# Kernel tuning notes

Measured on AMD Instinct MI355X. Metric: run time of the kernel, lower is better.

## Reference

```python
import jax, jax.numpy as jnp
import numpy as np

N = 100000   # total nodes (types a: [0,50000), b: [50000,100000))
E = 500000   # edges per edge type
T = 4        # number of edge types
D_IN = 128
H = 4        # heads
F = 32       # out_feats per head
NEG_SLOPE = 0.2


def setup_inputs() -> dict:
    key = jax.random.key(0)
    ks = jax.random.split(key, 8)
    feat = jax.random.normal(ks[0], (N, D_IN), dtype=jnp.float32)
    src = jax.random.randint(ks[1], (T, E), 0, N)
    dst = jax.random.randint(ks[2], (T, E), 0, N)
    is_b = jnp.arange(N) >= (N // 2)  # node-type mask (type2mask)
    W = jax.random.normal(ks[3], (T, D_IN, H * F), dtype=jnp.float32) * (1.0 / np.sqrt(D_IN))
    attn_l = jax.random.normal(ks[4], (T, H, F), dtype=jnp.float32) * 0.1
    attn_r = jax.random.normal(ks[5], (T, H, F), dtype=jnp.float32) * 0.1
    W_merge = jax.random.normal(ks[6], (2 * H * F, F), dtype=jnp.float32) * (1.0 / np.sqrt(2 * H * F))
    b_merge = jax.random.normal(ks[7], (F,), dtype=jnp.float32) * 0.01
    return {"feat": feat, "src": src, "dst": dst, "is_b": is_b,
            "W": W, "attn_l": attn_l, "attn_r": attn_r,
            "W_merge": W_merge, "b_merge": b_merge}


def _gat_etype(feat, src_t, dst_t, W_t, al_t, ar_t):
    # Projected features: [N, H, F]
    ft = (feat @ W_t).reshape(N, H, F)
    el = jnp.einsum('nhf,hf->nh', ft, al_t)  # [N, H]
    er = jnp.einsum('nhf,hf->nh', ft, ar_t)  # [N, H]
    # u_add_v then LeakyReLU: [E, H]
    e = el[src_t] + er[dst_t]
    e = jnp.where(e > 0, e, NEG_SLOPE * e)
    # edge_softmax over incoming edges of each dst node (stable)
    m = jax.lax.stop_gradient(jax.ops.segment_max(e, dst_t, num_segments=N))
    ex = jnp.exp(e - m[dst_t])
    denom = jax.ops.segment_sum(ex, dst_t, num_segments=N)
    a = ex / denom[dst_t]  # [E, H]
    # u_mul_e + scatter-sum: [N, H, F]
    msg = ft[src_t] * a[:, :, None]
    out = jax.ops.segment_sum(msg, dst_t, num_segments=N)
    return out.reshape(N, H * F)


def reference(feat, src, dst, is_b, W, attn_l, attn_r, W_merge, b_merge):
    outs = [_gat_etype(feat, src[t], dst[t], W[t], attn_l[t], attn_r[t])
            for t in range(T)]
    # etypes dst order: a, a, b, b -> two per-etype feats per dst ntype
    feat_a = jnp.concatenate([outs[0], outs[1]], axis=1) @ W_merge + b_merge  # [N, F]
    feat_b = jnp.concatenate([outs[2], outs[3]], axis=1) @ W_merge + b_merge  # [N, F]
    # base_aggr_func: start with type-a result, overwrite type-b rows
    return jnp.where(is_b[:, None], feat_b, feat_a)
```

## Files before the change

### kernel.cpp

```cpp
#include <hip/hip_runtime.h>
#include <hip/hip_fp16.h>

typedef short short8 __attribute__((ext_vector_type(8)));
typedef _Float16 half8 __attribute__((ext_vector_type(8)));
typedef float f32x4 __attribute__((ext_vector_type(4)));

#define N_NODES 100000
#define N_A     50000
#define N_EDGES 500000
#define N_T     4
#define D_IN    128
#define HF      128
#define BCOLS   144
#define TN      (N_T * N_NODES)
#define TE      (N_T * N_EDGES)
#define NB1     ((TN + 1023) / 1024)
#define TILE_E  (BCOLS * D_IN)
#define LOG2E   1.44269504088896340736f

__device__ __forceinline__ unsigned short f2b(float f) {
  unsigned int u = __float_as_uint(f);
  u += 0x7FFFu + ((u >> 16) & 1u);
  return (unsigned short)(u >> 16);
}
__device__ __forceinline__ unsigned int pkh(float lo, float hi) {
  auto v = __builtin_amdgcn_cvt_pkrtz(lo, hi);
  unsigned int u; __builtin_memcpy(&u, &v, 4); return u;
}
__device__ __forceinline__ unsigned short f2h(float f) {
  auto v = __builtin_amdgcn_cvt_pkrtz(f, 0.f);
  unsigned int u; __builtin_memcpy(&u, &v, 4); return (unsigned short)(u & 0xFFFFu);
}
__device__ __forceinline__ __half2 w2h(unsigned int u) {
  __half2 h; __builtin_memcpy(&h, &u, 4); return h;
}
__device__ __forceinline__ unsigned int h2w(__half2 h) {
  unsigned int u; __builtin_memcpy(&u, &h, 4); return u;
}

__global__ __launch_bounds__(256) void k_prep(const float* __restrict__ W,
    const float* __restrict__ al, const float* __restrict__ ar,
    const float* __restrict__ Wm,
    unsigned short* __restrict__ Bt, unsigned short* __restrict__ WmT)
{
  if (blockIdx.x < 2) {
    int idx = blockIdx.x * 256 + threadIdx.x;
    int t = idx >> 7, k = idx & 127;
    const float* Wr = W + ((size_t)t * D_IN + k) * HF;
    unsigned short* o = Bt + (size_t)t * TILE_E;
    for (int j = 0; j < HF; ++j)
      o[(j * D_IN + k) ^ ((j & 7) << 3)] = f2b(Wr[j]);
    for (int h = 0; h < 4; ++h) {
      float sl = 0.f, sr = 0.f;
      const float* alh = al + (t * 4 + h) * 32;
      const float* arh = ar + (t * 4 + h) * 32;
      for (int f = 0; f < 32; ++f) { float w = Wr[h * 32 + f]; sl += w * alh[f]; sr += w * arh[f]; }
      int jl = 128 + h, jr = 132 + h;
      o[(jl * D_IN + k) ^ ((jl & 7) << 3)] = f2b(sl * LOG2E);
      o[(jr * D_IN + k) ^ ((jr & 7) << 3)] = f2b(sr * LOG2E);
    }
    for (int j = 136; j < 144; ++j)
      o[(j * D_IN + k) ^ ((j & 7) << 3)] = 0;
  } else {
    int idx = (blockIdx.x - 2) * 256 + threadIdx.x;
    int kidx = idx >> 5, j = idx & 31;
    int slot = kidx >> 7, p = kidx & 127;
    int col = (p & 7) * 16 + (p >> 3);
    WmT[j * 256 + kidx] = f2h(Wm[(slot * 128 + col) * 32 + j]);
  }
}

__global__ __launch_bounds__(256, 4) void k_proj(const float* __restrict__ feat,
    const unsigned short* __restrict__ Btg,
    unsigned short* __restrict__ ftg,
    float* __restrict__ elg, float* __restrict__ erg)
{
  __shared__ __align__(16) unsigned short Bs[TILE_E];
  const int tid = threadIdx.x;
  const int wave = tid >> 6, lane = tid & 63;
  const int l15 = lane & 15, g = lane >> 4;
  const int wrow0 = blockIdx.x * 64 + wave * 16;

  short8 a[4];
  {
    int row = wrow0 + l15;
    const float* fr = feat + (size_t)(row < N_NODES ? row : N_NODES - 1) * D_IN;
#pragma unroll
    for (int kt = 0; kt < 4; ++kt) {
      float4 v0 = *(const float4*)(fr + kt * 32 + g * 8);
      float4 v1 = *(const float4*)(fr + kt * 32 + g * 8 + 4);
      short8 s;
      s[0] = (short)f2b(v0.x); s[1] = (short)f2b(v0.y);
      s[2] = (short)f2b(v0.z); s[3] = (short)f2b(v0.w);
      s[4] = (short)f2b(v1.x); s[5] = (short)f2b(v1.y);
      s[6] = (short)f2b(v1.z); s[7] = (short)f2b(v1.w);
      a[kt] = s;
    }
  }

  for (int t = 0; t < N_T; ++t) {
    if (t > 0) __syncthreads();
    {
      const uint4* src = (const uint4*)(Btg + (size_t)t * TILE_E);
      uint4* dstv = (uint4*)Bs;
#pragma unroll
      for (int i = 0; i < 9; ++i)
        dstv[i * 256 + tid] = src[i * 256 + tid];
    }
    __syncthreads();

    f32x4 acc[8];
#pragma unroll
    for (int ct = 0; ct < 8; ++ct) {
      f32x4 c = {0.f, 0.f, 0.f, 0.f};
#pragma unroll
      for (int kt = 0; kt < 4; ++kt) {
        int row = ct * 16 + l15;
        int boff = (row * 256 + kt * 64 + g * 16) ^ ((l15 & 7) << 4);
        short8 b = *(const short8*)((const char*)Bs + boff);
        c = __builtin_amdgcn_mfma_f32_16x16x32_bf16(a[kt], b, c, 0, 0, 0);
      }
      acc[ct] = c;
    }
    {
      f32x4 c8 = {0.f, 0.f, 0.f, 0.f};
#pragma unroll
      for (int kt = 0; kt < 4; ++kt) {
        int row = 128 + l15;
        int boff = (row * 256 + kt * 64 + g * 16) ^ ((l15 & 7) << 4);
        short8 b = *(const short8*)((const char*)Bs + boff);
        c8 = __builtin_amdgcn_mfma_f32_16x16x32_bf16(a[kt], b, c8, 0, 0, 0);
      }
      if (l15 < 8) {
#pragma unroll
        for (int r = 0; r < 4; ++r) {
          int row = wrow0 + g * 4 + r;
          if (row < N_NODES) {
            float v = c8[r];
            if (l15 < 4) elg[((size_t)t * N_NODES + row) * 4 + l15] = v;
            else         erg[((size_t)t * N_NODES + row) * 4 + (l15 - 4)] = v;
          }
        }
      }
    }
#pragma unroll
    for (int r = 0; r < 4; ++r) {
      int row = wrow0 + g * 4 + r;
      if (row < N_NODES) {
        uint4 o;
        o.x = pkh(acc[0][r], acc[1][r]);
        o.y = pkh(acc[2][r], acc[3][r]);
        o.z = pkh(acc[4][r], acc[5][r]);
        o.w = pkh(acc[6][r], acc[7][r]);
        *(uint4*)(ftg + ((size_t)t * N_NODES + row) * HF + l15 * 8) = o;
      }
    }
  }
}

__global__ __launch_bounds__(256) void k_hist(const int* __restrict__ dst,
    int* __restrict__ cnt, int* __restrict__ rank) {
  int idx = blockIdx.x * 256 + threadIdx.x;
  if (idx >= TE) return;
  int t = idx / N_EDGES;
  int d = dst[idx];
  bool keep = (t < 2) ? (d < N_A) : (d >= N_A);
  if (keep) rank[idx] = atomicAdd(&cnt[t * N_NODES + d], 1);
}

__global__ __launch_bounds__(256) void k_scan1(const int* __restrict__ cnt,
    int* __restrict__ ofs, int* __restrict__ bsum) {
  __shared__ int ts[256];
  int b = blockIdx.x, t = threadIdx.x;
  int base = b * 1024 + t * 4;
  int v0 = 0, v1 = 0, v2 = 0, v3 = 0;
  if (base + 0 < TN) v0 = cnt[base + 0];
  if (base + 1 < TN) v1 = cnt[base + 1];
  if (base + 2 < TN) v2 = cnt[base + 2];
  if (base + 3 < TN) v3 = cnt[base + 3];
  int s = v0 + v1 + v2 + v3;
  ts[t] = s;
  __syncthreads();
  for (int o = 1; o < 256; o <<= 1) {
    int x = (t >= o) ? ts[t - o] : 0;
    __syncthreads();
    ts[t] += x;
    __syncthreads();
  }
  int run = ts[t] - s;
  if (base + 0 < TN) ofs[base + 0] = run; run += v0;
  if (base + 1 < TN) ofs[base + 1] = run; run += v1;
  if (base + 2 < TN) ofs[base + 2] = run; run += v2;
  if (base + 3 < TN) ofs[base + 3] = run;
  if (t == 255) bsum[b] = ts[255];
}

__global__ __launch_bounds__(512) void k_scan2(int* __restrict__ bsum) {
  __shared__ int ts[512];
  int t = threadIdx.x;
  int v = (t < NB1) ? bsum[t] : 0;
  ts[t] = v;
  __syncthreads();
  for (int o = 1; o < 512; o <<= 1) {
    int x = (t >= o) ? ts[t - o] : 0;
    __syncthreads();
    ts[t] += x;
    __syncthreads();
  }
  if (t < NB1) bsum[t] = ts[t] - v;
}

__global__ __launch_bounds__(256) void k_scatter(const int* __restrict__ src, const int* __restrict__ dst,
    const int* __restrict__ ofs, const int* __restrict__ bsum, const int* __restrict__ rank,
    int* __restrict__ bkt) {
  int idx = blockIdx.x * 256 + threadIdx.x;
  if (idx >= TE) return;
  int t = idx / N_EDGES;
  int d = dst[idx];
  bool keep = (t < 2) ? (d < N_A) : (d >= N_A);
  if (!keep) return;
  int key = t * N_NODES + d;
  int p = ofs[key] + bsum[key >> 10] + rank[idx];
  bkt[p] = t * N_NODES + src[idx];
}

__global__ __launch_bounds__(256) void k_gathermerge(const int* __restrict__ bkt,
    const int* __restrict__ ofs, const int* __restrict__ cnt, const int* __restrict__ bsum,
    const float* __restrict__ elg, const float* __restrict__ erg,
    const uint4* __restrict__ ftu,
    const unsigned short* __restrict__ WmT, const float* __restrict__ bm,
    float* __restrict__ out)
{
  __shared__ __align__(16) unsigned short Al[16 * 264];
  int tid = threadIdx.x;
  int wave = tid >> 6, lane = tid & 63;
  int g8 = lane >> 3, l7 = lane & 7;
  int pidl = wave * 8 + g8;
  int pid = blockIdx.x * 32 + pidl;
  int n = pid >> 1, slot = pid & 1;
  int t = slot + ((n >= N_A) ? 2 : 0);
  int key = t * N_NODES + n;
  int base = ofs[key] + bsum[key >> 10];
  int c = cnt[key];
  float4 er4 = *(const float4*)(erg + (size_t)key * 4);
  __half2 A0 = __float2half2_rn(0.f), A1 = A0, A2 = A0, A3 = A0;
  __half2 B0 = A0, B1 = A0, B2 = A0, B3 = A0;
  float d0 = 0.f, d1 = 0.f, d2 = 0.f, d3 = 0.f;
  int qb = l7 * 2;
  for (int i = 0; i < c; i += 4) {
    bool v1 = i + 1 < c, v2 = i + 2 < c, v3 = i + 3 < c;
    int e0 = base + i;
    int e1 = base + (v1 ? i + 1 : i);
    int e2 = base + (v2 ? i + 2 : i);
    int e3 = base + (v3 ? i + 3 : i);
    int s0 = bkt[e0], s1 = bkt[e1], s2 = bkt[e2], s3 = bkt[e3];
    float4 eA = *(const float4*)(elg + (size_t)s0 * 4);
    float4 eB = *(const float4*)(elg + (size_t)s1 * 4);
    float4 eC = *(const float4*)(elg + (size_t)s2 * 4);
    float4 eD = *(const float4*)(elg + (size_t)s3 * 4);
    uint4 u0a = ftu[(size_t)s0 * 16 + qb], u0b = ftu[(size_t)s0 * 16 + qb + 1];
    uint4 u1a = ftu[(size_t)s1 * 16 + qb], u1b = ftu[(size_t)s1 * 16 + qb + 1];
    uint4 u2a = ftu[(size_t)s2 * 16 + qb], u2b = ftu[(size_t)s2 * 16 + qb + 1];
    uint4 u3a = ftu[(size_t)s3 * 16 + qb], u3b = ftu[(size_t)s3 * 16 + qb + 1];
    float s;
    float wa0, wa1, wa2, wa3, wb0, wb1, wb2, wb3;
    float wc0, wc1, wc2, wc3, wd0, wd1, wd2, wd3;
    s = eA.x + er4.x; wa0 = exp2f(fmaxf(s, 0.2f * s));
    s = eA.y + er4.y; wa1 = exp2f(fmaxf(s, 0.2f * s));
    s = eA.z + er4.z; wa2 = exp2f(fmaxf(s, 0.2f * s));
    s = eA.w + er4.w; wa3 = exp2f(fmaxf(s, 0.2f * s));
    s = eB.x + er4.x; wb0 = exp2f(fmaxf(s, 0.2f * s));
    s = eB.y + er4.y; wb1 = exp2f(fmaxf(s, 0.2f * s));
    s = eB.z + er4.z; wb2 = exp2f(fmaxf(s, 0.2f * s));
    s = eB.w + er4.w; wb3 = exp2f(fmaxf(s, 0.2f * s));
    s = eC.x + er4.x; wc0 = exp2f(fmaxf(s, 0.2f * s));
    s = eC.y + er4.y; wc1 = exp2f(fmaxf(s, 0.2f * s));
    s = eC.z + er4.z; wc2 = exp2f(fmaxf(s, 0.2f * s));
    s = eC.w + er4.w; wc3 = exp2f(fmaxf(s, 0.2f * s));
    s = eD.x + er4.x; wd0 = exp2f(fmaxf(s, 0.2f * s));
    s = eD.y + er4.y; wd1 = exp2f(fmaxf(s, 0.2f * s));
    s = eD.z + er4.z; wd2 = exp2f(fmaxf(s, 0.2f * s));
    s = eD.w + er4.w; wd3 = exp2f(fmaxf(s, 0.2f * s));
    if (!v1) { wb0 = wb1 = wb2 = wb3 = 0.f; }
    if (!v2) { wc0 = wc1 = wc2 = wc3 = 0.f; }
    if (!v3) { wd0 = wd1 = wd2 = wd3 = 0.f; }
    d0 += wa0 + wb0 + wc0 + wd0;
    d1 += wa1 + wb1 + wc1 + wd1;
    d2 += wa2 + wb2 + wc2 + wd2;
    d3 += wa3 + wb3 + wc3 + wd3;
    __half2 h0, h1, h2, h3;
    h0 = __float2half2_rn(wa0); h1 = __float2half2_rn(wa1);
    h2 = __float2half2_rn(wa2); h3 = __float2half2_rn(wa3);
    A0 = __hfma2(w2h(u0a.x), h0, A0); A1 = __hfma2(w2h(u0a.y), h1, A1);
    A2 = __hfma2(w2h(u0a.z), h2, A2); A3 = __hfma2(w2h(u0a.w), h3, A3);
    B0 = __hfma2(w2h(u0b.x), h0, B0); B1 = __hfma2(w2h(u0b.y), h1, B1);
    B2 = __hfma2(w2h(u0b.z), h2, B2); B3 = __hfma2(w2h(u0b.w), h3, B3);
    h0 = __float2half2_rn(wb0); h1 = __float2half2_rn(wb1);
    h2 = __float2half2_rn(wb2); h3 = __float2half2_rn(wb3);
    A0 = __hfma2(w2h(u1a.x), h0, A0); A1 = __hfma2(w2h(u1a.y), h1, A1);
    A2 = __hfma2(w2h(u1a.z), h2, A2); A3 = __hfma2(w2h(u1a.w), h3, A3);
    B0 = __hfma2(w2h(u1b.x), h0, B0); B1 = __hfma2(w2h(u1b.y), h1, B1);
    B2 = __hfma2(w2h(u1b.z), h2, B2); B3 = __hfma2(w2h(u1b.w), h3, B3);
    h0 = __float2half2_rn(wc0); h1 = __float2half2_rn(wc1);
    h2 = __float2half2_rn(wc2); h3 = __float2half2_rn(wc3);
    A0 = __hfma2(w2h(u2a.x), h0, A0); A1 = __hfma2(w2h(u2a.y), h1, A1);
    A2 = __hfma2(w2h(u2a.z), h2, A2); A3 = __hfma2(w2h(u2a.w), h3, A3);
    B0 = __hfma2(w2h(u2b.x), h0, B0); B1 = __hfma2(w2h(u2b.y), h1, B1);
    B2 = __hfma2(w2h(u2b.z), h2, B2); B3 = __hfma2(w2h(u2b.w), h3, B3);
    h0 = __float2half2_rn(wd0); h1 = __float2half2_rn(wd1);
    h2 = __float2half2_rn(wd2); h3 = __float2half2_rn(wd3);
    A0 = __hfma2(w2h(u3a.x), h0, A0); A1 = __hfma2(w2h(u3a.y), h1, A1);
    A2 = __hfma2(w2h(u3a.z), h2, A2); A3 = __hfma2(w2h(u3a.w), h3, A3);
    B0 = __hfma2(w2h(u3b.x), h0, B0); B1 = __hfma2(w2h(u3b.y), h1, B1);
    B2 = __hfma2(w2h(u3b.z), h2, B2); B3 = __hfma2(w2h(u3b.w), h3, B3);
  }
  __half2 i0 = __float2half2_rn((c > 0) ? 1.f / d0 : 0.f);
  __half2 i1 = __float2half2_rn((c > 0) ? 1.f / d1 : 0.f);
  __half2 i2 = __float2half2_rn((c > 0) ? 1.f / d2 : 0.f);
  __half2 i3 = __float2half2_rn((c > 0) ? 1.f / d3 : 0.f);
  uint4 oA, oB;
  oA.x = h2w(__hmul2(A0, i0)); oA.y = h2w(__hmul2(A1, i1));
  oA.z = h2w(__hmul2(A2, i2)); oA.w = h2w(__hmul2(A3, i3));
  oB.x = h2w(__hmul2(B0, i0)); oB.y = h2w(__hmul2(B1, i1));
  oB.z = h2w(__hmul2(B2, i2)); oB.w = h2w(__hmul2(B3, i3));
  int nl = pidl >> 1;
  *(uint4*)&Al[nl * 264 + slot * 128 + l7 * 16] = oA;
  *(uint4*)&Al[nl * 264 + slot * 128 + l7 * 16 + 8] = oB;
  __syncthreads();
  if (wave >= 2) return;

  int l15 = lane & 15, lk = (lane >> 4) * 8;
  f32x4 acc = {0.f, 0.f, 0.f, 0.f};
#pragma unroll
  for (int kt = 0; kt < 8; ++kt) {
    half8 a = *(const half8*)&Al[l15 * 264 + kt * 32 + lk];
    half8 b = *(const half8*)(const void*)(WmT + (size_t)(wave * 16 + l15) * 256 + kt * 32 + lk);
    acc = __builtin_amdgcn_mfma_f32_16x16x32_f16(a, b, acc, 0, 0, 0);
  }
  float bmv = bm[wave * 16 + l15];
#pragma unroll
  for (int r = 0; r < 4; ++r) {
    int row = blockIdx.x * 16 + (lane >> 4) * 4 + r;
    out[(size_t)row * 32 + wave * 16 + l15] = acc[r] + bmv;
  }
}

extern "C" void kernel_launch(void* const* d_in, const int* in_sizes, int n_in,
                              void* d_out, int out_size, void* d_ws, size_t ws_size,
                              hipStream_t stream)
{
  const float* feat = (const float*)d_in[0];
  const int*   src  = (const int*)d_in[1];
  const int*   dst  = (const int*)d_in[2];
  const float* W    = (const float*)d_in[4];
  const float* al   = (const float*)d_in[5];
  const float* ar   = (const float*)d_in[6];
  const float* Wm   = (const float*)d_in[7];
  const float* bm   = (const float*)d_in[8];
  float* out = (float*)d_out;
  (void)in_sizes; (void)n_in; (void)out_size; (void)ws_size;

  char* w = (char*)d_ws;
  size_t o = 0;
  auto take = [&](size_t bytes) -> void* {
    void* p = w + o;
    o += (bytes + 255) & ~(size_t)255;
    return p;
  };
  unsigned short* Btg = (unsigned short*)take((size_t)N_T * TILE_E * 2);
  unsigned short* WmT = (unsigned short*)take((size_t)32 * 256 * 2);
  unsigned short* ftg = (unsigned short*)take((size_t)N_T * N_NODES * HF * 2);
  float* elg   = (float*)take((size_t)N_T * N_NODES * 4 * 4);
  float* erg   = (float*)take((size_t)N_T * N_NODES * 4 * 4);
  int*   cntb  = (int*)take((size_t)TN * 4);
  int*   ofs   = (int*)take((size_t)TN * 4);
  int*   bsum  = (int*)take(4096);
  int*   rank  = (int*)take((size_t)TE * 4);
  int*   bkt   = (int*)take((size_t)TE * 4);

  hipMemsetAsync(cntb, 0, (size_t)TN * 4, stream);

  k_prep<<<34, 256, 0, stream>>>(W, al, ar, Wm, Btg, WmT);
  k_proj<<<1563, 256, 0, stream>>>(feat, Btg, ftg, elg, erg);
  k_hist<<<(TE + 255) / 256, 256, 0, stream>>>(dst, cntb, rank);
  k_scan1<<<NB1, 256, 0, stream>>>(cntb, ofs, bsum);
  k_scan2<<<1, 512, 0, stream>>>(bsum);
  k_scatter<<<(TE + 255) / 256, 256, 0, stream>>>(src, dst, ofs, bsum, rank, bkt);
  k_gathermerge<<<6250, 256, 0, stream>>>(bkt, ofs, cntb, bsum, elg, erg,
                                          (const uint4*)ftg, WmT, bm, out);
}
```

Measured before the change: 187.7 us.

## Fuse histogram, scans and scatter into one cooperative kernel; zero counts in prep

Replaces the four edge-bucketing kernels (hist, scan1, scan2, scatter) with a single cooperative kernel of 2048 blocks that uses grid-wide syncs between phases. The count buffer is now zeroed inside k_prep instead of with a separate memset. The aim is to cut launch overhead and inter-kernel gaps, at the price of grid.sync barriers and a grid-stride loop over fewer threads. The second-level scan now runs in one 256-thread block with two elements per thread.

```diff
diff --git a/kernel.cpp b/kernel.cpp
--- a/kernel.cpp
+++ b/kernel.cpp
@@ -1,5 +1,8 @@
 #include <hip/hip_runtime.h>
 #include <hip/hip_fp16.h>
+#include <hip/hip_cooperative_groups.h>
+
+namespace cg = cooperative_groups;
 
 typedef short short8 __attribute__((ext_vector_type(8)));
 typedef _Float16 half8 __attribute__((ext_vector_type(8)));
@@ -17,6 +20,7 @@
 #define NB1     ((TN + 1023) / 1024)
 #define TILE_E  (BCOLS * D_IN)
 #define LOG2E   1.44269504088896340736f
+#define SORTB   2048
 
 __device__ __forceinline__ unsigned short f2b(float f) {
   unsigned int u = __float_as_uint(f);
@@ -41,7 +45,8 @@
 __global__ __launch_bounds__(256) void k_prep(const float* __restrict__ W,
     const float* __restrict__ al, const float* __restrict__ ar,
     const float* __restrict__ Wm,
-    unsigned short* __restrict__ Bt, unsigned short* __restrict__ WmT)
+    unsigned short* __restrict__ Bt, unsigned short* __restrict__ WmT,
+    int* __restrict__ cnt)
 {
   if (blockIdx.x < 2) {
     int idx = blockIdx.x * 256 + threadIdx.x;
@@ -68,6 +73,8 @@
     int col = (p & 7) * 16 + (p >> 3);
     WmT[j * 256 + kidx] = f2h(Wm[(slot * 128 + col) * 32 + j]);
   }
+  for (int i = blockIdx.x * 256 + threadIdx.x; i < TN; i += 34 * 256)
+    cnt[i] = 0;
 }
 
 __global__ __launch_bounds__(256, 4) void k_proj(const float* __restrict__ feat,
@@ -158,70 +165,75 @@
   }
 }
 
-__global__ __launch_bounds__(256) void k_hist(const int* __restrict__ dst,
-    int* __restrict__ cnt, int* __restrict__ rank) {
-  int idx = blockIdx.x * 256 + threadIdx.x;
-  if (idx >= TE) return;
-  int t = idx / N_EDGES;
-  int d = dst[idx];
-  bool keep = (t < 2) ? (d < N_A) : (d >= N_A);
-  if (keep) rank[idx] = atomicAdd(&cnt[t * N_NODES + d], 1);
-}
-
-__global__ __launch_bounds__(256) void k_scan1(const int* __restrict__ cnt,
-    int* __restrict__ ofs, int* __restrict__ bsum) {
+__global__ __launch_bounds__(256, 8) void k_sort(const int* __restrict__ src,
+    const int* __restrict__ dst, int* __restrict__ cnt, int* __restrict__ rank,
+    int* __restrict__ ofs, int* __restrict__ bsum, int* __restrict__ bkt)
+{
+  cg::grid_group grid = cg::this_grid();
   __shared__ int ts[256];
-  int b = blockIdx.x, t = threadIdx.x;
-  int base = b * 1024 + t * 4;
-  int v0 = 0, v1 = 0, v2 = 0, v3 = 0;
-  if (base + 0 < TN) v0 = cnt[base + 0];
-  if (base + 1 < TN) v1 = cnt[base + 1];
-  if (base + 2 < TN) v2 = cnt[base + 2];
-  if (base + 3 < TN) v3 = cnt[base + 3];
-  int s = v0 + v1 + v2 + v3;
-  ts[t] = s;
-  __syncthreads();
-  for (int o = 1; o < 256; o <<= 1) {
-    int x = (t >= o) ? ts[t - o] : 0;
+  const int tid = threadIdx.x;
+  const int gtid = blockIdx.x * 256 + tid;
+
+  for (int idx = gtid; idx < TE; idx += SORTB * 256) {
+    int t = idx / N_EDGES;
+    int d = dst[idx];
+    bool keep = (t < 2) ? (d < N_A) : (d >= N_A);
+    if (keep) rank[idx] = atomicAdd(&cnt[t * N_NODES + d], 1);
+  }
+  grid.sync();
+
+  if (blockIdx.x < NB1) {
+    int base = blockIdx.x * 1024 + tid * 4;
+    int v0 = 0, v1 = 0, v2 = 0, v3 = 0;
+    if (base + 0 < TN) v0 = cnt[base + 0];
+    if (base + 1 < TN) v1 = cnt[base + 1];
+    if (base + 2 < TN) v2 = cnt[base + 2];
+    if (base + 3 < TN) v3 = cnt[base + 3];
+    int s = v0 + v1 + v2 + v3;
+    ts[tid] = s;
     __syncthreads();
-    ts[t] += x;
+    for (int o = 1; o < 256; o <<= 1) {
+      int x = (tid >= o) ? ts[tid - o] : 0;
+      __syncthreads();
+      ts[tid] += x;
+      __syncthreads();
+    }
+    int run = ts[tid] - s;
+    if (base + 0 < TN) ofs[base + 0] = run; run += v0;
+    if (base + 1 < TN) ofs[base + 1] = run; run += v1;
+    if (base + 2 < TN) ofs[base + 2] = run; run += v2;
+    if (base + 3 < TN) ofs[base + 3] = run;
+    if (tid == 255) bsum[blockIdx.x] = ts[255];
+  }
+  grid.sync();
+
+  if (blockIdx.x == 0) {
+    int a0 = (2 * tid < NB1) ? bsum[2 * tid] : 0;
+    int a1 = (2 * tid + 1 < NB1) ? bsum[2 * tid + 1] : 0;
+    int s = a0 + a1;
+    ts[tid] = s;
     __syncthreads();
-  }
-  int run = ts[t] - s;
-  if (base + 0 < TN) ofs[base + 0] = run; run += v0;
-  if (base + 1 < TN) ofs[base + 1] = run; run += v1;
-  if (base + 2 < TN) ofs[base + 2] = run; run += v2;
-  if (base + 3 < TN) ofs[base + 3] = run;
-  if (t == 255) bsum[b] = ts[255];
-}
-
-__global__ __launch_bounds__(512) void k_scan2(int* __restrict__ bsum) {
-  __shared__ int ts[512];
-  int t = threadIdx.x;
-  int v = (t < NB1) ? bsum[t] : 0;
-  ts[t] = v;
-  __syncthreads();
-  for (int o = 1; o < 512; o <<= 1) {
-    int x = (t >= o) ? ts[t - o] : 0;
-    __syncthreads();
-    ts[t] += x;
-    __syncthreads();
-  }
-  if (t < NB1) bsum[t] = ts[t] - v;
-}
-
-__global__ __launch_bounds__(256) void k_scatter(const int* __restrict__ src, const int* __restrict__ dst,
-    const int* __restrict__ ofs, const int* __restrict__ bsum, const int* __restrict__ rank,
-    int* __restrict__ bkt) {
-  int idx = blockIdx.x * 256 + threadIdx.x;
-  if (idx >= TE) return;
-  int t = idx / N_EDGES;
-  int d = dst[idx];
-  bool keep = (t < 2) ? (d < N_A) : (d >= N_A);
-  if (!keep) return;
-  int key = t * N_NODES + d;
-  int p = ofs[key] + bsum[key >> 10] + rank[idx];
-  bkt[p] = t * N_NODES + src[idx];
+    for (int o = 1; o < 256; o <<= 1) {
+      int x = (tid >= o) ? ts[tid - o] : 0;
+      __syncthreads();
+      ts[tid] += x;
+      __syncthreads();
+    }
+    int run = ts[tid] - s;
+    if (2 * tid < NB1) bsum[2 * tid] = run;
+    if (2 * tid + 1 < NB1) bsum[2 * tid + 1] = run + a0;
+  }
+  grid.sync();
+
+  for (int idx = gtid; idx < TE; idx += SORTB * 256) {
+    int t = idx / N_EDGES;
+    int d = dst[idx];
+    bool keep = (t < 2) ? (d < N_A) : (d >= N_A);
+    if (!keep) continue;
+    int key = t * N_NODES + d;
+    int p = ofs[key] + bsum[key >> 10] + rank[idx];
+    bkt[p] = t * N_NODES + src[idx];
+  }
 }
 
 __global__ __launch_bounds__(256) void k_gathermerge(const int* __restrict__ bkt,
@@ -369,23 +381,22 @@
   };
   unsigned short* Btg = (unsigned short*)take((size_t)N_T * TILE_E * 2);
   unsigned short* WmT = (unsigned short*)take((size_t)32 * 256 * 2);
-  unsigned short* ftg = (unsigned short*)take((size_t)N_T * N_NODES * HF * 2);
-  float* elg   = (float*)take((size_t)N_T * N_NODES * 4 * 4);
-  float* erg   = (float*)take((size_t)N_T * N_NODES * 4 * 4);
+  unsigned short* ftg = (unsigned short*)take((size_t)TN * HF * 2);
+  float* elg   = (float*)take((size_t)TN * 4 * 4);
+  float* erg   = (float*)take((size_t)TN * 4 * 4);
   int*   cntb  = (int*)take((size_t)TN * 4);
   int*   ofs   = (int*)take((size_t)TN * 4);
   int*   bsum  = (int*)take(4096);
   int*   rank  = (int*)take((size_t)TE * 4);
   int*   bkt   = (int*)take((size_t)TE * 4);
 
-  hipMemsetAsync(cntb, 0, (size_t)TN * 4, stream);
-
-  k_prep<<<34, 256, 0, stream>>>(W, al, ar, Wm, Btg, WmT);
+  k_prep<<<34, 256, 0, stream>>>(W, al, ar, Wm, Btg, WmT, cntb);
   k_proj<<<1563, 256, 0, stream>>>(feat, Btg, ftg, elg, erg);
-  k_hist<<<(TE + 255) / 256, 256, 0, stream>>>(dst, cntb, rank);
-  k_scan1<<<NB1, 256, 0, stream>>>(cntb, ofs, bsum);
-  k_scan2<<<1, 512, 0, stream>>>(bsum);
-  k_scatter<<<(TE + 255) / 256, 256, 0, stream>>>(src, dst, ofs, bsum, rank, bkt);
+  {
+    void* args[] = {(void*)&src, (void*)&dst, (void*)&cntb, (void*)&rank,
+                    (void*)&ofs, (void*)&bsum, (void*)&bkt};
+    hipLaunchCooperativeKernel((void*)k_sort, dim3(SORTB), dim3(256), args, 0, stream);
+  }
   k_gathermerge<<<6250, 256, 0, stream>>>(bkt, ofs, cntb, bsum, elg, erg,
                                           (const uint4*)ftg, WmT, bm, out);
 }
```

Result: slower. 737.9 us (+293.0%).
